# Performance work log

Hardware: AMD Instinct MI355X
Metric: run time of the kernel (lower is better)

The kernel has to match this reference:

```python
import jax, jax.numpy as jnp
import numpy as np

B, T, C, NH = 2, 2048, 1024, 16
HD = C // NH  # 64


def _ln(x, g, b, eps=1e-5):
    m = x.mean(-1, keepdims=True)
    v = ((x - m) ** 2).mean(-1, keepdims=True)
    return (x - m) / jnp.sqrt(v + eps) * g + b


def _ff(x, w1, b1, w2, b2):
    # Linear -> exact (erf) GELU -> Linear; dropout=0 (identity)
    return jax.nn.gelu(x @ w1 + b1, approximate=False) @ w2 + b2


def setup_inputs() -> dict:
    key = jax.random.key(0)
    ks = jax.random.split(key, 16)
    s = 0.02
    f32 = jnp.float32
    return {
        "x": jax.random.normal(ks[0], (B, T, C), f32),
        # SelfAttn qkv projection (torch Linear stored transposed: (in, out))
        "w_attn": jax.random.normal(ks[1], (C, 3 * C), f32) * s,
        "b_attn": jnp.zeros((3 * C,), f32),
        # SelfAttn's internal FeedForward
        "wa1": jax.random.normal(ks[2], (C, 4 * C), f32) * s,
        "ba1": jnp.zeros((4 * C,), f32),
        "wa2": jax.random.normal(ks[3], (4 * C, C), f32) * s,
        "ba2": jnp.zeros((C,), f32),
        # Block ln1
        "g1": jnp.ones((C,), f32),
        "be1": jnp.zeros((C,), f32),
        # Block FeedForward
        "wf1": jax.random.normal(ks[4], (C, 4 * C), f32) * s,
        "bf1": jnp.zeros((4 * C,), f32),
        "wf2": jax.random.normal(ks[5], (4 * C, C), f32) * s,
        "bf2": jnp.zeros((C,), f32),
        # Block ln2
        "g2": jnp.ones((C,), f32),
        "be2": jnp.zeros((C,), f32),
    }


def reference(x, w_attn, b_attn, wa1, ba1, wa2, ba2, g1, be1,
              wf1, bf1, wf2, bf2, g2, be2):
    Bx, Tx, Cx = x.shape
    qkv = x @ w_attn + b_attn  # (B, T, 3C)
    # NOTE: original splits as K, Q, V (in that order)
    K, Q, V = jnp.split(qkv, 3, axis=-1)

    def heads(t):  # (B, T, C) -> (B, NH, T, HD)
        return t.reshape(Bx, Tx, NH, HD).transpose(0, 2, 1, 3)

    Q, K, V = heads(Q), heads(K), heads(V)
    att = jnp.einsum('bhqd,bhkd->bhqk', Q, K) / np.float32(np.sqrt(HD))
    mask = jnp.tril(jnp.ones((Tx, Tx), bool))  # causal
    att = jnp.where(mask, att, -jnp.inf)
    att = jax.nn.softmax(att, axis=-1)
    y = jnp.einsum('bhqk,bhkd->bhqd', att, V)
    y = y.transpose(0, 2, 1, 3).reshape(Bx, Tx, Cx)
    # SelfAttn applies its own FeedForward (no output projection)
    y = _ff(y, wa1, ba1, wa2, ba2)
    # Block: post-sublayer LayerNorm, additive residuals
    x = x + _ln(y, g1, be1)
    x = x + _ln(_ff(x, wf1, bf1, wf2, bf2), g2, be2)
    return x
```

## Files before the change

kernel.cpp:

```cpp
#include <hip/hip_runtime.h>
#include <hip/hip_bf16.h>
#include <math.h>

#define Bz 2
#define Tz 2048
#define Cz 1024
#define NHz 16
#define HDz 64
#define Mz (Bz*Tz)

typedef unsigned short u16;
typedef __attribute__((ext_vector_type(8))) short bf16x8;
typedef __attribute__((ext_vector_type(4))) float f32x4;
typedef __attribute__((ext_vector_type(16))) float f32x16;

__device__ __forceinline__ float bf2f(u16 u){
  union { unsigned int i; float f; } v; v.i = ((unsigned int)u) << 16; return v.f;
}
__device__ __forceinline__ u16 f2bf(float f){
  union { float f; unsigned int i; } v; v.f = f;
  return (u16)((v.i + 0x7fffu + ((v.i >> 16) & 1u)) >> 16);
}
__device__ __forceinline__ unsigned pack_bf_trunc(float a, float b){
  union { float f; unsigned u; } ua, ub; ua.f = a; ub.f = b;
  return (ua.u >> 16) | (ub.u & 0xffff0000u);
}
__device__ __forceinline__ float gelu_fast(float x){
  float x3 = x * x * x;
  float z2 = 1.5957691216057308f * (x + 0.044715f * x3);
  float e  = __expf(z2);
  float t  = 1.f - 2.f / (e + 1.f);
  return 0.5f * x * (1.f + t);
}

__device__ __forceinline__ void glds16(const void* g, void* l){
  __builtin_amdgcn_global_load_lds(
      (const __attribute__((address_space(1))) void*)g,
      (__attribute__((address_space(3))) void*)l, 16, 0, 0);
}

__global__ __launch_bounds__(256) void cast4_kernel(const float* __restrict__ in,
                                                    u16* __restrict__ out, int n4){
  int i = blockIdx.x * 256 + threadIdx.x;
  if (i < n4) {
    float4 v = ((const float4*)in)[i];
    u16 t[4] = { f2bf(v.x), f2bf(v.y), f2bf(v.z), f2bf(v.w) };
    *(uint2*)&out[(size_t)i * 4] = *(const uint2*)t;
  }
}

__global__ __launch_bounds__(256) void transpose5_kernel(
    const float* __restrict__ s0, const float* __restrict__ s1,
    const float* __restrict__ s2, const float* __restrict__ s3,
    const float* __restrict__ s4,
    u16* __restrict__ d0, u16* __restrict__ d1, u16* __restrict__ d2,
    u16* __restrict__ d3, u16* __restrict__ d4){
  __shared__ float tile[32][33];
  const int t = blockIdx.x;
  const float* src; u16* dst; int K, N, local;
  if (t < 3072)       { src = s0; dst = d0; K = 1024; N = 3072; local = t; }
  else if (t < 7168)  { src = s1; dst = d1; K = 1024; N = 4096; local = t - 3072; }
  else if (t < 11264) { src = s2; dst = d2; K = 4096; N = 1024; local = t - 7168; }
  else if (t < 15360) { src = s3; dst = d3; K = 1024; N = 4096; local = t - 11264; }
  else                { src = s4; dst = d4; K = 4096; N = 1024; local = t - 15360; }
  const int NT = N >> 5;
  const int kb = (local / NT) * 32, nb = (local % NT) * 32;
  const int tx = threadIdx.x & 31, ty = threadIdx.x >> 5;
  #pragma unroll
  for (int r = ty; r < 32; r += 8)
    tile[r][tx] = src[(size_t)(kb + r) * N + nb + tx];
  __syncthreads();
  #pragma unroll
  for (int r = ty; r < 32; r += 8)
    dst[(size_t)(nb + r) * K + kb + tx] = f2bf(tile[tx][r]);
}

template<int ACT>
__global__ __launch_bounds__(256) void gemm_kernel(const u16* __restrict__ A,
                                                   const u16* __restrict__ Bt,
                                                   const float* __restrict__ bias,
                                                   u16* __restrict__ ob0,
                                                   u16* __restrict__ ob1,
                                                   int N, int lda, int klen){
  __shared__ __align__(16) u16 As[2][128 * 32];
  __shared__ __align__(16) u16 Bs[2][128 * 32];
  const int tid  = threadIdx.x;
  const int wave = tid >> 6, lane = tid & 63;
  const int wm = (wave & 1) * 64, wn = (wave >> 1) * 64;
  const int m0 = blockIdx.x * 128, n0 = blockIdx.y * 128;
  const int kz = blockIdx.z;
  const int l31 = lane & 31, h8 = (lane >> 5) * 8;

  const u16* Ak  = A  + (size_t)kz * klen;
  const u16* Btk = Bt + (size_t)kz * klen;

  f32x16 acc[2][2] = {};

  const int nk = klen / 64;
  for (int ki = 0; ki < nk; ki++) {
    const int k0 = ki * 64;
    __syncthreads();
    #pragma unroll
    for (int it = 0; it < 4; it++) {
      int ci = tid + it * 256;
      int half = ci >> 9, rem = ci & 511;
      int row = rem >> 2, c4 = rem & 3;
      int gofs = k0 + half * 32 + c4 * 8;
      glds16(Ak  + (size_t)(m0 + row) * lda + gofs, &As[half][row * 32 + c4 * 8]);
      glds16(Btk + (size_t)(n0 + row) * lda + gofs, &Bs[half][row * 32 + c4 * 8]);
    }
    __syncthreads();

    #pragma unroll
    for (int p = 0; p < 2; p++) {
      bf16x8 af[2][2], bfr[2][2];
      #pragma unroll
      for (int mt = 0; mt < 2; mt++)
        #pragma unroll
        for (int s = 0; s < 2; s++) {
          af[mt][s]  = *(const bf16x8*)&As[p][(wm + mt * 32 + l31) * 32 + s * 16 + h8];
          bfr[mt][s] = *(const bf16x8*)&Bs[p][(wn + mt * 32 + l31) * 32 + s * 16 + h8];
        }
      #pragma unroll
      for (int s = 0; s < 2; s++)
        #pragma unroll
        for (int mt = 0; mt < 2; mt++)
          #pragma unroll
          for (int nt = 0; nt < 2; nt++)
            acc[mt][nt] = __builtin_amdgcn_mfma_f32_32x32x16_bf16(
                af[mt][s], bfr[nt][s], acc[mt][nt], 0, 0, 0);
    }
  }

  const float* bias_k = (kz == 0) ? bias : nullptr;
  u16* ob = (kz == 0) ? ob0 : ob1;
  const int rql = 4 * (lane >> 5);
  #pragma unroll
  for (int mt = 0; mt < 2; mt++) {
    #pragma unroll
    for (int nt = 0; nt < 2; nt++) {
      int col = n0 + wn + nt * 32 + l31;
      float bv = bias_k ? bias_k[col] : 0.f;
      #pragma unroll
      for (int reg = 0; reg < 16; reg++) {
        int row = m0 + wm + mt * 32 + rql + (reg & 3) + 8 * (reg >> 2);
        float v = acc[mt][nt][reg] + bv;
        if (ACT == 1) v = gelu_fast(v);
        ob[(size_t)row * N + col] = f2bf(v);
      }
    }
  }
}

__global__ __launch_bounds__(256) void vtrans_kernel(const u16* __restrict__ qkv,
                                                     u16* __restrict__ Vtb){
  __shared__ u16 Vl[64 * 72];
  const int tid = threadIdx.x;
  const int t0 = blockIdx.x * 64, h = blockIdx.y, b = blockIdx.z;
  const int bh = b * NHz + h;
  #pragma unroll
  for (int it = 0; it < 2; it++) {
    int c = tid + it * 256;
    int row = c >> 3, g = c & 7;
    *(uint4*)&Vl[row * 72 + g * 8] =
        *(const uint4*)(qkv + (size_t)(b * Tz + t0 + row) * (3 * Cz) + 2 * Cz + h * 64 + g * 8);
  }
  __syncthreads();
  #pragma unroll
  for (int it = 0; it < 2; it++) {
    int c = tid + it * 256;
    int d = c >> 3, tg = c & 7;
    u16 tmp[8];
    #pragma unroll
    for (int e = 0; e < 8; e++) tmp[e] = Vl[(tg * 8 + e) * 72 + d];
    *(uint4*)&Vtb[((size_t)bh * 64 + d) * Tz + t0 + tg * 8] = *(const uint4*)tmp;
  }
}

__global__ __launch_bounds__(256) void attn_kernel(const u16* __restrict__ qkv,
                                                   const u16* __restrict__ Vtb,
                                                   u16* __restrict__ y){
  __shared__ __align__(16) u16 KV[2][2][64 * 64];
  __shared__ __align__(16) u16 Ps[64 * 72];
  const int tid = threadIdx.x;
  const int lane = tid & 63, wave = tid >> 6;
  const int cc = lane & 15, quad = lane >> 4;
  const int h = blockIdx.y, b = blockIdx.z;
  const int bh = b * NHz + h;
  const size_t rowb = (size_t)b * Tz;
  const int wq0 = wave * 16;

  int foff[4][2];
  const int sw0 = (quad ^ (cc & 7)) * 8;
  const int sw1 = ((4 + quad) ^ (cc & 7)) * 8;
  #pragma unroll
  for (int t = 0; t < 4; ++t) {
    foff[t][0] = (t * 16 + cc) * 64 + sw0;
    foff[t][1] = (t * 16 + cc) * 64 + sw1;
  }
  const int pswb = (wq0 + cc) * 72 + quad * 4;
  const int psr0 = (wq0 + cc) * 72 + quad * 8;
  const int psr1 = (wq0 + cc) * 72 + 32 + quad * 8;

  auto stage = [&](int i, int bsel) {
    const int k0s = i * 64;
    #pragma unroll
    for (int it = 0; it < 2; ++it) {
      int ci = tid + it * 256;
      int row = ci >> 3, g = ci & 7;
      int gs = g ^ (row & 7);
      glds16(qkv + (rowb + k0s + row) * (3 * Cz) + h * 64 + gs * 8, &KV[bsel][0][ci * 8]);
      glds16(Vtb + ((size_t)bh * 64 + row) * Tz + k0s + gs * 8,     &KV[bsel][1][ci * 8]);
    }
  };

  for (int ph = 0; ph < 2; ++ph) {
    const int qt = ph ? (31 - (int)blockIdx.x) : (int)blockIdx.x;
    const int q0t = qt * 64 + wq0;
    const int nkt = qt + 1;
    const int wqmax = q0t + 15;

    bf16x8 qf[2];
    #pragma unroll
    for (int s = 0; s < 2; ++s)
      qf[s] = *(const bf16x8*)(qkv + (rowb + q0t + cc) * (3 * Cz)
                               + Cz + h * 64 + s * 32 + quad * 8);
    f32x4 acc[4] = {};
    float lp = 0.f;

    if (ph) __syncthreads();
    stage(0, 0);

    for (int i = 0; i < nkt; ++i) {
      __syncthreads();
      if (i + 1 < nkt) stage(i + 1, (i + 1) & 1);
      const int sel = i & 1;
      const u16* Kl = KV[sel][0];
      const u16* Vl = KV[sel][1];
      const int k0 = i * 64;
      if (k0 > wqmax) continue;

      bf16x8 kf[4][2];
      #pragma unroll
      for (int kt = 0; kt < 4; ++kt) {
        kf[kt][0] = *(const bf16x8*)&Kl[foff[kt][0]];
        kf[kt][1] = *(const bf16x8*)&Kl[foff[kt][1]];
      }
      const int qbase = q0t;
      #pragma unroll
      for (int kt = 0; kt < 4; ++kt) {
        const int kbase = k0 + kt * 16;
        uint2 pk;
        if (kbase > qbase + 15) {
          pk.x = 0u; pk.y = 0u;
        } else {
          f32x4 st = __builtin_amdgcn_mfma_f32_16x16x32_bf16(
              kf[kt][0], qf[0], (f32x4){0.f, 0.f, 0.f, 0.f}, 0, 0, 0);
          st = __builtin_amdgcn_mfma_f32_16x16x32_bf16(kf[kt][1], qf[1], st, 0, 0, 0);
          if (kbase + 15 > qbase) {
            const int kq = kbase + quad * 4, ql = qbase + cc;
            st[0] = (kq     <= ql) ? st[0] : -1e30f;
            st[1] = (kq + 1 <= ql) ? st[1] : -1e30f;
            st[2] = (kq + 2 <= ql) ? st[2] : -1e30f;
            st[3] = (kq + 3 <= ql) ? st[3] : -1e30f;
          }
          float p0 = __expf(fmaf(st[0], 0.125f, -16.f));
          float p1 = __expf(fmaf(st[1], 0.125f, -16.f));
          float p2 = __expf(fmaf(st[2], 0.125f, -16.f));
          float p3 = __expf(fmaf(st[3], 0.125f, -16.f));
          lp += (p0 + p1) + (p2 + p3);
          pk.x = pack_bf_trunc(p0, p1);
          pk.y = pack_bf_trunc(p2, p3);
        }
        *(uint2*)&Ps[pswb + kt * 16] = pk;
      }
      bf16x8 pf0 = *(const bf16x8*)&Ps[psr0];
      bf16x8 pf1 = *(const bf16x8*)&Ps[psr1];
      #pragma unroll
      for (int jd = 0; jd < 4; ++jd) {
        bf16x8 vf0 = *(const bf16x8*)&Vl[foff[jd][0]];
        bf16x8 vf1 = *(const bf16x8*)&Vl[foff[jd][1]];
        acc[jd] = __builtin_amdgcn_mfma_f32_16x16x32_bf16(pf0, vf0, acc[jd], 0, 0, 0);
        acc[jd] = __builtin_amdgcn_mfma_f32_16x16x32_bf16(pf1, vf1, acc[jd], 0, 0, 0);
      }
    }

    lp += __shfl_xor(lp, 16, 64);
    lp += __shfl_xor(lp, 32, 64);
    float inv[4];
    #pragma unroll
    for (int r = 0; r < 4; ++r) inv[r] = 1.f / __shfl(lp, quad * 4 + r, 64);
    #pragma unroll
    for (int jd = 0; jd < 4; ++jd)
      #pragma unroll
      for (int r = 0; r < 4; ++r) {
        int qrow = q0t + quad * 4 + r;
        y[(rowb + qrow) * Cz + h * 64 + jd * 16 + cc] = f2bf(acc[jd][r] * inv[r]);
      }
  }
}

__global__ __launch_bounds__(256) void ln_resid_kernel(const float* __restrict__ x,
                                                       const u16* __restrict__ y1,
                                                       const u16* __restrict__ y2,
                                                       const float* __restrict__ g,
                                                       const float* __restrict__ be,
                                                       float* __restrict__ outf,
                                                       u16* __restrict__ outb){
  const int row = blockIdx.x;
  const int c0 = threadIdx.x * 4;
  const size_t base = (size_t)row * Cz + c0;
  uint2 p1 = *(const uint2*)(y1 + base);
  float4 v;
  v.x = bf2f((u16)(p1.x & 0xffff)); v.y = bf2f((u16)(p1.x >> 16));
  v.z = bf2f((u16)(p1.y & 0xffff)); v.w = bf2f((u16)(p1.y >> 16));
  if (y2) {
    uint2 p2 = *(const uint2*)(y2 + base);
    v.x += bf2f((u16)(p2.x & 0xffff)); v.y += bf2f((u16)(p2.x >> 16));
    v.z += bf2f((u16)(p2.y & 0xffff)); v.w += bf2f((u16)(p2.y >> 16));
  }
  float s  = v.x + v.y + v.z + v.w;
  float s2 = v.x*v.x + v.y*v.y + v.z*v.z + v.w*v.w;
  #pragma unroll
  for (int off = 32; off > 0; off >>= 1) {
    s  += __shfl_down(s,  off);
    s2 += __shfl_down(s2, off);
  }
  __shared__ float ps[4], ps2[4];
  int wave = threadIdx.x >> 6, lane = threadIdx.x & 63;
  if (lane == 0) { ps[wave] = s; ps2[wave] = s2; }
  __syncthreads();
  s  = ps[0]  + ps[1]  + ps[2]  + ps[3];
  s2 = ps2[0] + ps2[1] + ps2[2] + ps2[3];
  const float mean = s * (1.f / Cz);
  const float var  = s2 * (1.f / Cz) - mean * mean;
  const float rstd = rsqrtf(var + 1e-5f);
  float4 xv = *(const float4*)(x + base);
  float4 gv = *(const float4*)(g + c0);
  float4 bv = *(const float4*)(be + c0);
  float4 ov;
  ov.x = xv.x + (v.x - mean) * rstd * gv.x + bv.x;
  ov.y = xv.y + (v.y - mean) * rstd * gv.y + bv.y;
  ov.z = xv.z + (v.z - mean) * rstd * gv.z + bv.z;
  ov.w = xv.w + (v.w - mean) * rstd * gv.w + bv.w;
  *(float4*)(outf + base) = ov;
  if (outb) {
    u16 t[4] = { f2bf(ov.x), f2bf(ov.y), f2bf(ov.z), f2bf(ov.w) };
    *(ulonglong1*)&outb[base] = *(const ulonglong1*)t;
  }
}

extern "C" void kernel_launch(void* const* d_in, const int* in_sizes, int n_in,
                              void* d_out, int out_size, void* d_ws, size_t ws_size,
                              hipStream_t stream) {
  const float* x      = (const float*)d_in[0];
  const float* w_attn = (const float*)d_in[1];
  const float* b_attn = (const float*)d_in[2];
  const float* wa1    = (const float*)d_in[3];
  const float* ba1    = (const float*)d_in[4];
  const float* wa2    = (const float*)d_in[5];
  const float* ba2    = (const float*)d_in[6];
  const float* g1     = (const float*)d_in[7];
  const float* be1    = (const float*)d_in[8];
  const float* wf1    = (const float*)d_in[9];
  const float* bf1    = (const float*)d_in[10];
  const float* wf2    = (const float*)d_in[11];
  const float* bf2    = (const float*)d_in[12];
  const float* g2     = (const float*)d_in[13];
  const float* be2    = (const float*)d_in[14];
  float* out = (float*)d_out;

  char* ws = (char*)d_ws;
  size_t off = 0;
  auto alloc = [&](size_t bytes) { size_t o = off; off += (bytes + 255) & ~(size_t)255; return o; };
  u16* qkvb    = (u16*)(ws + alloc((size_t)Mz * 3 * Cz * 2));
  u16* ybuf    = (u16*)(ws + alloc((size_t)Mz * Cz * 2));
  u16* xb      = (u16*)(ws + alloc((size_t)Mz * Cz * 2));
  u16* wT_attn = (u16*)(ws + alloc((size_t)3 * Cz * Cz * 2));
  u16* wT_a1   = (u16*)(ws + alloc((size_t)4 * Cz * Cz * 2));
  u16* Vtb     = (u16*)(ws + alloc((size_t)Bz * NHz * HDz * Tz * 2));
  u16* wT_a2   = (u16*)(ws + alloc((size_t)4 * Cz * Cz * 2));
  u16* wT_f1   = (u16*)(ws + alloc((size_t)4 * Cz * Cz * 2));
  u16* wT_f2   = (u16*)(ws + alloc((size_t)4 * Cz * Cz * 2));
  u16* hbuf    = (u16*)(ws + alloc((size_t)Mz * 4 * Cz * 2));
  u16* pb0     = (u16*)(ws + alloc((size_t)Mz * Cz * 2));
  u16* pb1     = (u16*)(ws + alloc((size_t)Mz * Cz * 2));
  float* x1f   = (float*)(ws + alloc((size_t)Mz * Cz * 4));
  u16* x1b     = (u16*)(ws + alloc((size_t)Mz * Cz * 2));
  alloc(256);
  (void)ws_size; (void)in_sizes; (void)n_in; (void)out_size;

  cast4_kernel<<<(Mz * Cz / 4 + 255) / 256, 256, 0, stream>>>(x, xb, Mz * Cz / 4);
  transpose5_kernel<<<19456, 256, 0, stream>>>(w_attn, wa1, wa2, wf1, wf2,
                                               wT_attn, wT_a1, wT_a2, wT_f1, wT_f2);

  gemm_kernel<0><<<dim3(Mz/128, 3*Cz/128, 1), 256, 0, stream>>>(xb, wT_attn, b_attn,
      qkvb, nullptr, 3*Cz, Cz, Cz);

  vtrans_kernel<<<dim3(Tz/64, NHz, Bz), 256, 0, stream>>>(qkvb, Vtb);
  attn_kernel<<<dim3(16, NHz, Bz), 256, 0, stream>>>(qkvb, Vtb, ybuf);

  gemm_kernel<1><<<dim3(Mz/128, 4*Cz/128, 1), 256, 0, stream>>>(ybuf, wT_a1, ba1,
      hbuf, nullptr, 4*Cz, Cz, Cz);
  gemm_kernel<0><<<dim3(Mz/128, Cz/128, 2), 256, 0, stream>>>(hbuf, wT_a2, ba2,
      pb0, pb1, Cz, 4*Cz, 2*Cz);

  ln_resid_kernel<<<Mz, 256, 0, stream>>>(x, pb0, pb1, g1, be1, x1f, x1b);

  gemm_kernel<1><<<dim3(Mz/128, 4*Cz/128, 1), 256, 0, stream>>>(x1b, wT_f1, bf1,
      hbuf, nullptr, 4*Cz, Cz, Cz);
  gemm_kernel<0><<<dim3(Mz/128, Cz/128, 2), 256, 0, stream>>>(hbuf, wT_f2, bf2,
      pb0, pb1, Cz, 4*Cz, 2*Cz);

  ln_resid_kernel<<<Mz, 256, 0, stream>>>(x1f, pb0, pb1, g2, be2, out, nullptr);
}
```

Baseline: 484.3 us.

## Switch GEMM to 16x16x32 MFMA tiles and drop fp32 residual buffer

The GEMM inner loop moves from 32x32x16 MFMA with 2x2 tiles per wave to 16x16x32 MFMA with 4x4 tiles per wave. This changes the LDS fragment access pattern and the epilogue store layout. The second change drops the fp32 intermediate residual x1f: the first LayerNorm writes only the bf16 copy, and the final LayerNorm reads the residual from bf16. That cuts memory traffic but rounds the residual path to bf16, which lowers accuracy.

```diff
diff --git a/kernel.cpp b/kernel.cpp
--- a/kernel.cpp
+++ b/kernel.cpp
@@ -12,7 +12,6 @@
 typedef unsigned short u16;
 typedef __attribute__((ext_vector_type(8))) short bf16x8;
 typedef __attribute__((ext_vector_type(4))) float f32x4;
-typedef __attribute__((ext_vector_type(16))) float f32x16;
 
 __device__ __forceinline__ float bf2f(u16 u){
   union { unsigned int i; float f; } v; v.i = ((unsigned int)u) << 16; return v.f;
@@ -89,12 +88,13 @@
   const int wm = (wave & 1) * 64, wn = (wave >> 1) * 64;
   const int m0 = blockIdx.x * 128, n0 = blockIdx.y * 128;
   const int kz = blockIdx.z;
-  const int l31 = lane & 31, h8 = (lane >> 5) * 8;
+  const int cc = lane & 15, quad = lane >> 4;
+  const int lko = quad * 8;
 
   const u16* Ak  = A  + (size_t)kz * klen;
   const u16* Btk = Bt + (size_t)kz * klen;
 
-  f32x16 acc[2][2] = {};
+  f32x4 acc[4][4] = {};
 
   const int nk = klen / 64;
   for (int ki = 0; ki < nk; ki++) {
@@ -112,39 +112,35 @@
     __syncthreads();
 
     #pragma unroll
-    for (int p = 0; p < 2; p++) {
-      bf16x8 af[2][2], bfr[2][2];
-      #pragma unroll
-      for (int mt = 0; mt < 2; mt++)
+    for (int s = 0; s < 2; s++) {
+      bf16x8 af[4], bfr[4];
+      #pragma unroll
+      for (int i = 0; i < 4; i++)
+        af[i]  = *(const bf16x8*)&As[s][(wm + i * 16 + cc) * 32 + lko];
+      #pragma unroll
+      for (int j = 0; j < 4; j++)
+        bfr[j] = *(const bf16x8*)&Bs[s][(wn + j * 16 + cc) * 32 + lko];
+      #pragma unroll
+      for (int i = 0; i < 4; i++)
         #pragma unroll
-        for (int s = 0; s < 2; s++) {
-          af[mt][s]  = *(const bf16x8*)&As[p][(wm + mt * 32 + l31) * 32 + s * 16 + h8];
-          bfr[mt][s] = *(const bf16x8*)&Bs[p][(wn + mt * 32 + l31) * 32 + s * 16 + h8];
-        }
-      #pragma unroll
-      for (int s = 0; s < 2; s++)
-        #pragma unroll
-        for (int mt = 0; mt < 2; mt++)
-          #pragma unroll
-          for (int nt = 0; nt < 2; nt++)
-            acc[mt][nt] = __builtin_amdgcn_mfma_f32_32x32x16_bf16(
-                af[mt][s], bfr[nt][s], acc[mt][nt], 0, 0, 0);
+        for (int j = 0; j < 4; j++)
+          acc[i][j] = __builtin_amdgcn_mfma_f32_16x16x32_bf16(af[i], bfr[j], acc[i][j], 0, 0, 0);
     }
   }
 
   const float* bias_k = (kz == 0) ? bias : nullptr;
   u16* ob = (kz == 0) ? ob0 : ob1;
-  const int rql = 4 * (lane >> 5);
-  #pragma unroll
-  for (int mt = 0; mt < 2; mt++) {
-    #pragma unroll
-    for (int nt = 0; nt < 2; nt++) {
-      int col = n0 + wn + nt * 32 + l31;
+  const int rbase = quad * 4;
+  #pragma unroll
+  for (int i = 0; i < 4; i++) {
+    #pragma unroll
+    for (int j = 0; j < 4; j++) {
+      int col = n0 + wn + j * 16 + cc;
       float bv = bias_k ? bias_k[col] : 0.f;
       #pragma unroll
-      for (int reg = 0; reg < 16; reg++) {
-        int row = m0 + wm + mt * 32 + rql + (reg & 3) + 8 * (reg >> 2);
-        float v = acc[mt][nt][reg] + bv;
+      for (int r = 0; r < 4; r++) {
+        int row = m0 + wm + i * 16 + rbase + r;
+        float v = acc[i][j][r] + bv;
         if (ACT == 1) v = gelu_fast(v);
         ob[(size_t)row * N + col] = f2bf(v);
       }
@@ -300,7 +296,8 @@
   }
 }
 
-__global__ __launch_bounds__(256) void ln_resid_kernel(const float* __restrict__ x,
+__global__ __launch_bounds__(256) void ln_resid_kernel(const float* __restrict__ xf,
+                                                       const u16* __restrict__ xb16,
                                                        const u16* __restrict__ y1,
                                                        const u16* __restrict__ y2,
                                                        const float* __restrict__ g,
@@ -335,7 +332,14 @@
   const float mean = s * (1.f / Cz);
   const float var  = s2 * (1.f / Cz) - mean * mean;
   const float rstd = rsqrtf(var + 1e-5f);
-  float4 xv = *(const float4*)(x + base);
+  float4 xv;
+  if (xf) {
+    xv = *(const float4*)(xf + base);
+  } else {
+    uint2 px = *(const uint2*)(xb16 + base);
+    xv.x = bf2f((u16)(px.x & 0xffff)); xv.y = bf2f((u16)(px.x >> 16));
+    xv.z = bf2f((u16)(px.y & 0xffff)); xv.w = bf2f((u16)(px.y >> 16));
+  }
   float4 gv = *(const float4*)(g + c0);
   float4 bv = *(const float4*)(be + c0);
   float4 ov;
@@ -343,7 +347,7 @@
   ov.y = xv.y + (v.y - mean) * rstd * gv.y + bv.y;
   ov.z = xv.z + (v.z - mean) * rstd * gv.z + bv.z;
   ov.w = xv.w + (v.w - mean) * rstd * gv.w + bv.w;
-  *(float4*)(outf + base) = ov;
+  if (outf) *(float4*)(outf + base) = ov;
   if (outb) {
     u16 t[4] = { f2bf(ov.x), f2bf(ov.y), f2bf(ov.z), f2bf(ov.w) };
     *(ulonglong1*)&outb[base] = *(const ulonglong1*)t;
@@ -385,7 +389,6 @@
   u16* hbuf    = (u16*)(ws + alloc((size_t)Mz * 4 * Cz * 2));
   u16* pb0     = (u16*)(ws + alloc((size_t)Mz * Cz * 2));
   u16* pb1     = (u16*)(ws + alloc((size_t)Mz * Cz * 2));
-  float* x1f   = (float*)(ws + alloc((size_t)Mz * Cz * 4));
   u16* x1b     = (u16*)(ws + alloc((size_t)Mz * Cz * 2));
   alloc(256);
   (void)ws_size; (void)in_sizes; (void)n_in; (void)out_size;
@@ -405,12 +408,14 @@
   gemm_kernel<0><<<dim3(Mz/128, Cz/128, 2), 256, 0, stream>>>(hbuf, wT_a2, ba2,
       pb0, pb1, Cz, 4*Cz, 2*Cz);
 
-  ln_resid_kernel<<<Mz, 256, 0, stream>>>(x, pb0, pb1, g1, be1, x1f, x1b);
+  ln_resid_kernel<<<Mz, 256, 0, stream>>>(x, nullptr, pb0, pb1, g1, be1,
+                                          nullptr, x1b);
 
   gemm_kernel<1><<<dim3(Mz/128, 4*Cz/128, 1), 256, 0, stream>>>(x1b, wT_f1, bf1,
       hbuf, nullptr, 4*Cz, Cz, Cz);
   gemm_kernel<0><<<dim3(Mz/128, Cz/128, 2), 256, 0, stream>>>(hbuf, wT_f2, bf2,
       pb0, pb1, Cz, 4*Cz, 2*Cz);
 
-  ln_resid_kernel<<<Mz, 256, 0, stream>>>(x1f, pb0, pb1, g2, be2, out, nullptr);
-}
+  ln_resid_kernel<<<Mz, 256, 0, stream>>>(nullptr, x1b, pb0, pb1, g2, be2,
+                                          out, nullptr);
+}
```

Result: no change. 481.3 us (-0.6%).
